# Performance work log

Hardware: AMD Instinct MI355X
Metric: run time of the kernel (lower is better)

Reference implementation:

```python
import jax, jax.numpy as jnp
import numpy as np

H = 512      # number of independent SSM copies (model width)
N2 = 32      # N // 2 : half state size (conjugate pairs)
CHANNELS = 1
RANK = 1
LENGTH = 2048


def setup_inputs() -> dict:
    key = jax.random.key(0)
    ks = jax.random.split(key, 6)
    # log_dt ~ Uniform[log(dt_min), log(dt_max)]
    log_dt = jax.random.uniform(ks[0], (H,), jnp.float32) * (np.log(0.1) - np.log(0.001)) + np.log(0.001)
    # w = -exp(log_w_real) + i * w_imag ; HiPPO-legs-like init (real part ~ -0.5, imag ~ pi*n)
    log_w_real = jnp.full((H, N2), np.log(0.5), jnp.float32) + 0.1 * jax.random.normal(ks[1], (H, N2), jnp.float32)
    w_imag = jnp.broadcast_to(np.pi * jnp.arange(N2, dtype=np.float32), (H, N2)) + 0.1 * jax.random.normal(ks[2], (H, N2), jnp.float32)
    B = jax.random.normal(ks[3], (H, N2, 2), jnp.float32)
    C = jax.random.normal(ks[4], (CHANNELS, H, N2, 2), jnp.float32)
    P = 0.3 * jax.random.normal(ks[5], (RANK, H, N2, 2), jnp.float32)
    return {"log_dt": log_dt, "log_w_real": log_w_real, "w_imag": w_imag,
            "B": B, "C": C, "P": P, "L": LENGTH}


def reference(log_dt, log_w_real, w_imag, B, C, P, L):
    """S4 SSKernelNPLR forward: generate conv kernel k of shape (channels, H, L).

    Math (state-spaces S4 NPLR kernel, rank-1 Woodbury):
      dt = exp(log_dt); w = -exp(log_w_real) + i w_imag
      nodes: omega_m = exp(-2 pi i m / L), z = 2(1-omega)/(1+omega)  (bilinear)
      r[a,b,h,m] = dt_h * sum_n (Bf[a] Cf[b])_n / (z_m - dt_h * w_{h,n})   (Cauchy, conj pairs)
      k_f = (r_BC - r_BQ r_PC / (1 + r_PQ)) * 2/(1+omega);  k = irfft(k_f, L)
    """
    w = -jnp.exp(log_w_real) + 1j * w_imag                       # (H, N2)
    Bc = (B[..., 0] + 1j * B[..., 1])[None]                      # (1, H, N2)
    Cc = C[..., 0] + 1j * C[..., 1]                              # (c, H, N2)
    Pc = P[..., 0] + 1j * P[..., 1]                              # (r, H, N2)
    Qc = Pc.conj()
    dt = jnp.exp(log_dt)                                         # (H,)

    M = L // 2 + 1
    omega = jnp.exp(-2j * jnp.pi * jnp.arange(M) / L)            # (M,) FFT nodes
    z = 2 * (1 - omega) / (1 + omega)                            # bilinear-transformed nodes

    w_dt = w * dt[:, None]                                       # incorporate dt into A

    Bf = jnp.concatenate([Bc, Pc], axis=0)                       # (1+r, H, N2)
    Cf = jnp.concatenate([Cc, Qc], axis=0)                       # (c+r, H, N2)
    v = Bf[:, None] * Cf[None]                                   # (1+r, c+r, H, N2)

    # conjugate-pair expansion (handles the implicit conjugate half of the spectrum)
    v_ = jnp.concatenate([v, v.conj()], axis=-1)                 # (1+r, c+r, H, 2*N2)
    w_ = jnp.concatenate([w_dt, w_dt.conj()], axis=-1)           # (H, 2*N2)

    # Cauchy kernel: r[a,b,h,m] = sum_n v[a,b,h,n] / (z[m] - w[h,n])
    den = 1.0 / (z[None, :, None] - w_[:, None, :])              # (H, M, 2*N2)
    r = jnp.einsum('abhn,hmn->abhm', v_, den)                    # (1+r, c+r, H, M)
    r = r * dt[None, None, :, None]

    # rank-1 Woodbury low-rank correction
    k_f = r[:-1, :-1] - r[:-1, -1:] * r[-1:, :-1] / (1.0 + r[-1:, -1:])   # (1, c, H, M)
    k_f = k_f * 2.0 / (1.0 + omega)

    k = jnp.fft.irfft(k_f, n=L, axis=-1)                         # (1, c, H, L)
    return k[-1]                                                 # (c, H, L)
```

## Files before the change

kernel.cpp:

```cpp
#include <hip/hip_runtime.h>
#include <math.h>

#ifndef M_PI
#define M_PI 3.14159265358979323846
#endif

#define NPOLE 32
#define SLEN 2048
#define NHALF 1024

__global__ __launch_bounds__(256) void s4_nplr_kernel(
    const float* __restrict__ g_log_dt,
    const float* __restrict__ g_log_w_real,
    const float* __restrict__ g_w_imag,
    const float* __restrict__ g_B,
    const float* __restrict__ g_C,
    const float* __restrict__ g_P,
    float* __restrict__ g_out)
{
    const int h   = blockIdx.x;
    const int tid = threadIdx.x;

    __shared__ float4 sA[NPOLE];
    __shared__ float4 sB[NPOLE];
    __shared__ float  sC[NPOLE];
    __shared__ __align__(16) float2 bufA[NHALF];
    __shared__ __align__(16) float2 bufB[NHALF];
    __shared__ float2 stw[512];
    __shared__ float2 s_kf_last;

    const float dt = expf(g_log_dt[h]);

    if (tid < NPOLE) {
        const int n   = tid;
        const int idx = h * NPOLE + n;
        const float ar  = expf(g_log_w_real[idx]) * dt;
        const float wim = g_w_imag[idx] * dt;
        const float Br = g_B[2*idx+0], Bi = g_B[2*idx+1];
        const float Cr = g_C[2*idx+0], Ci = g_C[2*idx+1];
        const float Pr = g_P[2*idx+0], Pi = g_P[2*idx+1];
        sA[n] = make_float4(ar, wim, dt*(Br*Cr - Bi*Ci), dt*(Br*Ci + Bi*Cr));
        sB[n] = make_float4(dt*(Br*Pr + Bi*Pi), dt*(Bi*Pr - Br*Pi),
                            dt*(Pr*Cr - Pi*Ci), dt*(Pr*Ci + Pi*Cr));
        sC[n] = dt*(Pr*Pr + Pi*Pi);
    }
    for (int k = tid; k < 512; k += 256) {
        float ang = (float)(M_PI / 512.0) * (float)k;
        float sn, cs;
        sincosf(ang, &sn, &cs);
        stw[k] = make_float2(cs, sn);
    }
    __syncthreads();

    float tj[4], t2[4];
    #pragma unroll
    for (int j = 0; j < 4; ++j) {
        tj[j] = tanf((float)(tid + (j << 8)) * (float)(M_PI / 2048.0));
        t2[j] = tj[j] + tj[j];
    }
    float acc[4][8];
    #pragma unroll
    for (int j = 0; j < 4; ++j)
        #pragma unroll
        for (int q = 0; q < 8; ++q) acc[j][q] = 0.0f;

    #pragma unroll 2
    for (int n = 0; n < NPOLE; ++n) {
        const float4 a  = sA[n];
        const float4 b  = sB[n];
        const float v11 = sC[n];
        const float ar = a.x, wim = a.y;
        const float ar2 = ar * ar;
        #pragma unroll
        for (int j = 0; j < 4; ++j) {
            float aim = t2[j] - wim, aip = t2[j] + wim;
            float inv1 = __builtin_amdgcn_rcpf(fmaf(aim, aim, ar2));
            float inv2 = __builtin_amdgcn_rcpf(fmaf(aip, aip, ar2));
            float d1r = ar * inv1,   e2r = ar * inv2;
            float d1i = -aim * inv1, e2i = -aip * inv2;
            float Sr = d1r + e2r, Dr = d1r - e2r;
            float Si = d1i + e2i, Di = e2i - d1i;
            acc[j][0] = fmaf(a.z, Sr, fmaf(a.w, Di, acc[j][0]));
            acc[j][1] = fmaf(a.z, Si, fmaf(a.w, Dr, acc[j][1]));
            acc[j][2] = fmaf(b.x, Sr, fmaf(b.y, Di, acc[j][2]));
            acc[j][3] = fmaf(b.x, Si, fmaf(b.y, Dr, acc[j][3]));
            acc[j][4] = fmaf(b.z, Sr, fmaf(b.w, Di, acc[j][4]));
            acc[j][5] = fmaf(b.z, Si, fmaf(b.w, Dr, acc[j][5]));
            acc[j][6] = fmaf(v11, Sr, acc[j][6]);
            acc[j][7] = fmaf(v11, Si, acc[j][7]);
        }
    }

    #pragma unroll
    for (int j = 0; j < 4; ++j) {
        float wdr = 1.0f + acc[j][6], wdi = acc[j][7];
        float winv = __builtin_amdgcn_rcpf(fmaf(wdr, wdr, wdi*wdi));
        float trm = acc[j][2]*acc[j][4] - acc[j][3]*acc[j][5];
        float tim = acc[j][2]*acc[j][5] + acc[j][3]*acc[j][4];
        float cr = (trm*wdr + tim*wdi) * winv;
        float ci = (tim*wdr - trm*wdi) * winv;
        float kr = acc[j][0] - cr, ki = acc[j][1] - ci;
        bufA[tid + (j << 8)] = make_float2(fmaf(-ki, tj[j], kr), fmaf(kr, tj[j], ki));
    }
    if (tid == 0) {
        float s = 0.0f;
        #pragma unroll
        for (int n = 0; n < NPOLE; ++n) s += sA[n].z;
        s_kf_last = make_float2(s, 0.0f);
    }
    __syncthreads();

    #pragma unroll
    for (int jj = 0; jj < 4; ++jj) {
        const int l = tid + (jj << 8);
        float2 Xm = bufA[l];
        float2 Xn = (l == 0) ? s_kf_last : bufA[NHALF - l];
        if (l == 0) { Xm.y = 0.0f; Xn.y = 0.0f; }
        float er  = 0.5f*(Xm.x + Xn.x);
        float ei  = 0.5f*(Xm.y - Xn.y);
        float odr = 0.5f*(Xm.x - Xn.x);
        float odi = 0.5f*(Xm.y + Xn.y);
        float ang = (float)(M_PI/1024.0) * (float)l;
        float sn, cs;
        sincosf(ang, &sn, &cs);
        float Or = odr*cs - odi*sn;
        float Oi = odr*sn + odi*cs;
        bufB[l] = make_float2(er - Oi, ei + Or);
    }
    __syncthreads();

    float2* src = bufB;
    float2* dst = bufA;
    int s = 1;
    for (int t = 0; t < 10; ++t) {
        #pragma unroll
        for (int j = 0; j < 2; ++j) {
            const int i    = tid + (j << 8);
            const int lo   = i & (s - 1);
            const int base = i - lo;
            float2 twf = stw[base];
            float2 a = src[i];
            float2 b = src[i + 512];
            float2 sum = make_float2(a.x + b.x, a.y + b.y);
            float2 dif = make_float2(a.x - b.x, a.y - b.y);
            float2 tw  = make_float2(dif.x*twf.x - dif.y*twf.y,
                                     dif.x*twf.y + dif.y*twf.x);
            const int o = base*2 + lo;
            dst[o]     = sum;
            dst[o + s] = tw;
        }
        __syncthreads();
        float2* tmp = src; src = dst; dst = tmp;
        s <<= 1;
    }

    const float scale = 1.0f / (float)NHALF;
    float4* outp = (float4*)(g_out + (size_t)h * SLEN);
    #pragma unroll
    for (int l = tid; l < 512; l += 256) {
        const float4 y2 = *((const float4*)&src[2*l]);
        outp[l] = make_float4(y2.x*scale, y2.y*scale, y2.z*scale, y2.w*scale);
    }
}

extern "C" void kernel_launch(void* const* d_in, const int* in_sizes, int n_in,
                              void* d_out, int out_size, void* d_ws, size_t ws_size,
                              hipStream_t stream) {
    const float* log_dt     = (const float*)d_in[0];
    const float* log_w_real = (const float*)d_in[1];
    const float* w_imag     = (const float*)d_in[2];
    const float* B          = (const float*)d_in[3];
    const float* C          = (const float*)d_in[4];
    const float* P          = (const float*)d_in[5];
    float* out = (float*)d_out;
    const int H = in_sizes[0];
    s4_nplr_kernel<<<H, 256, 0, stream>>>(log_dt, log_w_real, w_imag, B, C, P, out);
}
```

Baseline: 84.53 us.

## Split fused S4 kernel into pole, Cauchy, and IFFT kernels via workspace

Splits the single per-channel kernel into three launches: a pole-precompute kernel writing coefficient tables to workspace, a Cauchy kernel using four times as many blocks with one frequency per thread, and an IFFT kernel reading the spectrum from global memory. The aim is more parallelism and lower register pressure in the Cauchy stage, so occupancy rises across the GPU. In exchange it adds two extra launches and a round trip of the spectrum through global memory.

Result: slower. 88.84 us (+5.1%).

```diff
diff --git a/kernel.cpp b/kernel.cpp
--- a/kernel.cpp
+++ b/kernel.cpp
@@ -9,113 +9,121 @@
 #define SLEN 2048
 #define NHALF 1024
 
-__global__ __launch_bounds__(256) void s4_nplr_kernel(
+__global__ __launch_bounds__(64) void s4_pole_kernel(
     const float* __restrict__ g_log_dt,
     const float* __restrict__ g_log_w_real,
     const float* __restrict__ g_w_imag,
     const float* __restrict__ g_B,
     const float* __restrict__ g_C,
     const float* __restrict__ g_P,
-    float* __restrict__ g_out)
+    float4* __restrict__ tabA,
+    float4* __restrict__ tabB,
+    float*  __restrict__ tabC,
+    float*  __restrict__ nyq)
 {
-    const int h   = blockIdx.x;
-    const int tid = threadIdx.x;
-
-    __shared__ float4 sA[NPOLE];
-    __shared__ float4 sB[NPOLE];
-    __shared__ float  sC[NPOLE];
-    __shared__ __align__(16) float2 bufA[NHALF];
-    __shared__ __align__(16) float2 bufB[NHALF];
-    __shared__ float2 stw[512];
-    __shared__ float2 s_kf_last;
-
+    const int h = blockIdx.x;
+    const int n = threadIdx.x;
     const float dt = expf(g_log_dt[h]);
-
-    if (tid < NPOLE) {
-        const int n   = tid;
+    float s = 0.0f;
+    if (n < NPOLE) {
         const int idx = h * NPOLE + n;
         const float ar  = expf(g_log_w_real[idx]) * dt;
         const float wim = g_w_imag[idx] * dt;
         const float Br = g_B[2*idx+0], Bi = g_B[2*idx+1];
         const float Cr = g_C[2*idx+0], Ci = g_C[2*idx+1];
         const float Pr = g_P[2*idx+0], Pi = g_P[2*idx+1];
-        sA[n] = make_float4(ar, wim, dt*(Br*Cr - Bi*Ci), dt*(Br*Ci + Bi*Cr));
-        sB[n] = make_float4(dt*(Br*Pr + Bi*Pi), dt*(Bi*Pr - Br*Pi),
-                            dt*(Pr*Cr - Pi*Ci), dt*(Pr*Ci + Pi*Cr));
-        sC[n] = dt*(Pr*Pr + Pi*Pi);
-    }
+        const float v00r = dt*(Br*Cr - Bi*Ci);
+        tabA[idx] = make_float4(ar, wim, v00r, dt*(Br*Ci + Bi*Cr));
+        tabB[idx] = make_float4(dt*(Br*Pr + Bi*Pi), dt*(Bi*Pr - Br*Pi),
+                                dt*(Pr*Cr - Pi*Ci), dt*(Pr*Ci + Pi*Cr));
+        tabC[idx] = dt*(Pr*Pr + Pi*Pi);
+        s = v00r;
+    }
+    #pragma unroll
+    for (int off = 32; off > 0; off >>= 1) s += __shfl_down(s, off);
+    if (n == 0) nyq[h] = s;
+}
+
+__global__ __launch_bounds__(256) void s4_cauchy_kernel(
+    const float4* __restrict__ tabA,
+    const float4* __restrict__ tabB,
+    const float*  __restrict__ tabC,
+    float2* __restrict__ kf)
+{
+    const int h = blockIdx.x >> 2;
+    const int m = ((blockIdx.x & 3) << 8) | threadIdx.x;
+    const float4* __restrict__ pA = tabA + h * NPOLE;
+    const float4* __restrict__ pB = tabB + h * NPOLE;
+    const float*  __restrict__ pC = tabC + h * NPOLE;
+
+    const float t  = tanf((float)m * (float)(M_PI / 2048.0));
+    const float t2 = t + t;
+
+    float r00r=0.f, r00i=0.f, r01r=0.f, r01i=0.f;
+    float r10r=0.f, r10i=0.f, r11r=0.f, r11i=0.f;
+
+    #pragma unroll 8
+    for (int n = 0; n < NPOLE; ++n) {
+        const float4 a  = pA[n];
+        const float4 b  = pB[n];
+        const float v11 = pC[n];
+        const float ar = a.x, wim = a.y;
+        const float ar2 = ar * ar;
+        float aim = t2 - wim, aip = t2 + wim;
+        float inv1 = __builtin_amdgcn_rcpf(fmaf(aim, aim, ar2));
+        float inv2 = __builtin_amdgcn_rcpf(fmaf(aip, aip, ar2));
+        float d1r = ar * inv1,   e2r = ar * inv2;
+        float d1i = -aim * inv1, e2i = -aip * inv2;
+        float Sr = d1r + e2r, Dr = d1r - e2r;
+        float Si = d1i + e2i, Di = e2i - d1i;
+        r00r = fmaf(a.z, Sr, fmaf(a.w, Di, r00r));
+        r00i = fmaf(a.z, Si, fmaf(a.w, Dr, r00i));
+        r01r = fmaf(b.x, Sr, fmaf(b.y, Di, r01r));
+        r01i = fmaf(b.x, Si, fmaf(b.y, Dr, r01i));
+        r10r = fmaf(b.z, Sr, fmaf(b.w, Di, r10r));
+        r10i = fmaf(b.z, Si, fmaf(b.w, Dr, r10i));
+        r11r = fmaf(v11, Sr, r11r);
+        r11i = fmaf(v11, Si, r11i);
+    }
+
+    float wdr = 1.0f + r11r, wdi = r11i;
+    float winv = __builtin_amdgcn_rcpf(fmaf(wdr, wdr, wdi*wdi));
+    float trm = r01r*r10r - r01i*r10i;
+    float tim = r01r*r10i + r01i*r10r;
+    float cr = (trm*wdr + tim*wdi) * winv;
+    float ci = (tim*wdr - trm*wdi) * winv;
+    float kr = r00r - cr, ki = r00i - ci;
+    kf[h * NHALF + m] = make_float2(fmaf(-ki, t, kr), fmaf(kr, t, ki));
+}
+
+__global__ __launch_bounds__(256) void s4_ifft_kernel(
+    const float2* __restrict__ kf,
+    const float*  __restrict__ nyq,
+    float* __restrict__ g_out)
+{
+    const int h   = blockIdx.x;
+    const int tid = threadIdx.x;
+
+    __shared__ __align__(16) float2 bufA[NHALF];
+    __shared__ __align__(16) float2 bufB[NHALF];
+    __shared__ float2 stw[512];
+
+    const float2* __restrict__ X = kf + (size_t)h * NHALF;
+    const float nyqv = nyq[h];
+
     for (int k = tid; k < 512; k += 256) {
         float ang = (float)(M_PI / 512.0) * (float)k;
         float sn, cs;
         sincosf(ang, &sn, &cs);
         stw[k] = make_float2(cs, sn);
     }
-    __syncthreads();
-
-    float tj[4], t2[4];
-    #pragma unroll
-    for (int j = 0; j < 4; ++j) {
-        tj[j] = tanf((float)(tid + (j << 8)) * (float)(M_PI / 2048.0));
-        t2[j] = tj[j] + tj[j];
-    }
-    float acc[4][8];
-    #pragma unroll
-    for (int j = 0; j < 4; ++j)
-        #pragma unroll
-        for (int q = 0; q < 8; ++q) acc[j][q] = 0.0f;
-
-    #pragma unroll 2
-    for (int n = 0; n < NPOLE; ++n) {
-        const float4 a  = sA[n];
-        const float4 b  = sB[n];
-        const float v11 = sC[n];
-        const float ar = a.x, wim = a.y;
-        const float ar2 = ar * ar;
-        #pragma unroll
-        for (int j = 0; j < 4; ++j) {
-            float aim = t2[j] - wim, aip = t2[j] + wim;
-            float inv1 = __builtin_amdgcn_rcpf(fmaf(aim, aim, ar2));
-            float inv2 = __builtin_amdgcn_rcpf(fmaf(aip, aip, ar2));
-            float d1r = ar * inv1,   e2r = ar * inv2;
-            float d1i = -aim * inv1, e2i = -aip * inv2;
-            float Sr = d1r + e2r, Dr = d1r - e2r;
-            float Si = d1i + e2i, Di = e2i - d1i;
-            acc[j][0] = fmaf(a.z, Sr, fmaf(a.w, Di, acc[j][0]));
-            acc[j][1] = fmaf(a.z, Si, fmaf(a.w, Dr, acc[j][1]));
-            acc[j][2] = fmaf(b.x, Sr, fmaf(b.y, Di, acc[j][2]));
-            acc[j][3] = fmaf(b.x, Si, fmaf(b.y, Dr, acc[j][3]));
-            acc[j][4] = fmaf(b.z, Sr, fmaf(b.w, Di, acc[j][4]));
-            acc[j][5] = fmaf(b.z, Si, fmaf(b.w, Dr, acc[j][5]));
-            acc[j][6] = fmaf(v11, Sr, acc[j][6]);
-            acc[j][7] = fmaf(v11, Si, acc[j][7]);
-        }
-    }
-
-    #pragma unroll
-    for (int j = 0; j < 4; ++j) {
-        float wdr = 1.0f + acc[j][6], wdi = acc[j][7];
-        float winv = __builtin_amdgcn_rcpf(fmaf(wdr, wdr, wdi*wdi));
-        float trm = acc[j][2]*acc[j][4] - acc[j][3]*acc[j][5];
-        float tim = acc[j][2]*acc[j][5] + acc[j][3]*acc[j][4];
-        float cr = (trm*wdr + tim*wdi) * winv;
-        float ci = (tim*wdr - trm*wdi) * winv;
-        float kr = acc[j][0] - cr, ki = acc[j][1] - ci;
-        bufA[tid + (j << 8)] = make_float2(fmaf(-ki, tj[j], kr), fmaf(kr, tj[j], ki));
-    }
-    if (tid == 0) {
-        float s = 0.0f;
-        #pragma unroll
-        for (int n = 0; n < NPOLE; ++n) s += sA[n].z;
-        s_kf_last = make_float2(s, 0.0f);
-    }
-    __syncthreads();
 
     #pragma unroll
     for (int jj = 0; jj < 4; ++jj) {
         const int l = tid + (jj << 8);
-        float2 Xm = bufA[l];
-        float2 Xn = (l == 0) ? s_kf_last : bufA[NHALF - l];
-        if (l == 0) { Xm.y = 0.0f; Xn.y = 0.0f; }
+        float2 Xm = X[l];
+        float2 Xn = (l == 0) ? make_float2(nyqv, 0.0f) : X[NHALF - l];
+        if (l == 0) Xm.y = 0.0f;
         float er  = 0.5f*(Xm.x + Xn.x);
         float ei  = 0.5f*(Xm.y - Xn.y);
         float odr = 0.5f*(Xm.x - Xn.x);
@@ -172,7 +180,22 @@
     const float* B          = (const float*)d_in[3];
     const float* C          = (const float*)d_in[4];
     const float* P          = (const float*)d_in[5];
-    float* out = (float*)d_out;
     const int H = in_sizes[0];
-    s4_nplr_kernel<<<H, 256, 0, stream>>>(log_dt, log_w_real, w_imag, B, C, P, out);
-}
+
+    char* ws = (char*)d_ws;
+    size_t offA = 0;
+    size_t offB = offA + (size_t)H * NPOLE * 16;
+    size_t offC = offB + (size_t)H * NPOLE * 16;
+    size_t offN = offC + (size_t)H * NPOLE * 4;
+    size_t offK = offN + (((size_t)H * 4 + 15) & ~15ull);
+    float4* tabA = (float4*)(ws + offA);
+    float4* tabB = (float4*)(ws + offB);
+    float*  tabC = (float*)(ws + offC);
+    float*  nyq  = (float*)(ws + offN);
+    float2* kf   = (float2*)(ws + offK);
+
+    s4_pole_kernel<<<H, 64, 0, stream>>>(log_dt, log_w_real, w_imag, B, C, P,
+                                         tabA, tabB, tabC, nyq);
+    s4_cauchy_kernel<<<H * 4, 256, 0, stream>>>(tabA, tabB, tabC, kf);
+    s4_ifft_kernel<<<H, 256, 0, stream>>>(kf, nyq, (float*)d_out);
+}
```
